# Optimization experiments

Hardware: AMD Instinct MI355X
Metric: run time of the kernel (lower is better)

The kernel has to match this reference:

```python
import jax, jax.numpy as jnp
import numpy as np

NFFT = 640
HOP = 320
REF_CH = 3  # reference microphone index


def _hann(n):
    # periodic Hann, matches torch.hann_window(n)
    return 0.5 * (1.0 - jnp.cos(2.0 * jnp.pi * jnp.arange(n, dtype=jnp.float32) / n))


def _stft(x):
    # x: [..., T] -> complex [..., F, Tf], center=True, constant (zero) pad
    win = _hann(NFFT)
    pad = NFFT // 2
    xp = jnp.pad(x, [(0, 0)] * (x.ndim - 1) + [(pad, pad)])
    T = x.shape[-1]
    nf = 1 + T // HOP
    idx = jnp.arange(nf)[:, None] * HOP + jnp.arange(NFFT)[None, :]
    frames = xp[..., idx] * win  # [..., Tf, NFFT]
    return jnp.swapaxes(jnp.fft.rfft(frames, axis=-1), -1, -2)  # [..., F, Tf]


def _istft(S):
    # S: [..., F, Tf] complex -> real [..., (Tf-1)*HOP]
    win = _hann(NFFT)
    frames = jnp.fft.irfft(jnp.swapaxes(S, -1, -2), n=NFFT, axis=-1) * win
    Tf = S.shape[-1]
    L = (Tf - 1) * HOP + NFFT
    idx = jnp.arange(Tf)[:, None] * HOP + jnp.arange(NFFT)[None, :]
    out = jnp.zeros(S.shape[:-2] + (L,), frames.dtype).at[..., idx].add(frames)
    wsum = jnp.zeros((L,), frames.dtype).at[idx].add(win * win)
    out = out / jnp.where(wsum > 1e-11, wsum, 1.0)
    p = NFFT // 2
    return out[..., p:L - p]


def _cov_features(xb):
    # xb: [C, T] -> [C*(C+1) + 2, F, Tf]
    S = _stft(xb)  # [C, F, Tf] complex
    C = xb.shape[0]
    iu, ju = np.triu_indices(C)  # upper triangle, row-major (matches torch mask order)
    cov = S[iu] * jnp.conj(S[ju])  # [C*(C+1)/2, F, Tf], cov[i,j] = S_i * conj(S_j)
    nF, nT = S.shape[-2], S.shape[-1]
    cov_ri = jnp.stack([cov.real, cov.imag], axis=1).reshape(-1, nF, nT)  # interleave re/im
    ref = S[REF_CH]
    return jnp.concatenate([cov_ri, ref.real[None], ref.imag[None]], axis=0)


def _forward(x, rtf_g, ref_g):
    B, C, T = x.shape
    feats = jax.vmap(_cov_features)(x)  # [B, 74, F, Tf]
    # STFT of generated reference channel
    refS = _stft(ref_g.reshape(B, -1))  # [B, F, Tf] complex
    nF, nT = refS.shape[-2], refS.shape[-1]
    # deep-filtering: unfold kernel (3,9) with padding (1,4) over (freq, frame)
    rp = jnp.pad(refS, ((0, 0), (1, 1), (4, 4)))
    patches = jnp.stack([rp[:, ki:ki + nF, kj:kj + nT]
                         for ki in range(3) for kj in range(9)], axis=1)  # [B, 27, F, Tf]
    rtf_c = (rtf_g[..., 0] + 1j * rtf_g[..., 1]).reshape(B, C - 1, 27, nF, nT)
    est = jnp.einsum('bmkft,bkft->bmft', rtf_c, patches)  # [B, C-1, F, Tf]
    est_audio = _istft(est.reshape(B * (C - 1), nF, nT)).reshape(B, C - 1, -1)
    valid = min(est_audio.shape[-1], ref_g.shape[-1])
    all_ch = jnp.concatenate([est_audio[:, :REF_CH, :valid],
                              ref_g[..., :valid],
                              est_audio[:, REF_CH:, :valid]], axis=1)  # [B, C, valid]
    return all_ch[0].T, feats


def setup_inputs() -> dict:
    key = jax.random.key(0)
    k1, k2, k3 = jax.random.split(key, 3)
    B, C, T = 2, 8, 96000
    nF, nT = NFFT // 2 + 1, 1 + T // HOP  # 321, 301
    x = jax.random.normal(k1, (B, C, T), dtype=jnp.float32)
    rtf_g = jax.random.normal(k2, (B, C - 1, 3, 9, nF, nT, 2), dtype=jnp.float32) * 0.1
    ref_g = jax.random.normal(k3, (B, 1, T), dtype=jnp.float32)
    return {"x": x, "rtf_g": rtf_g, "ref_g": ref_g}


def reference(x, rtf_g, ref_g):
    return _forward(x, rtf_g, ref_g)
```

## Files before the change

kernel.cpp:

```cpp
#include <hip/hip_runtime.h>
#include <math.h>

#define TLEN 96000
#define NFFT 640
#define HOP  320
#define NF   321
#define NT   301
#define FT   (NF * NT)

#define TWO_PI_F 6.28318530717958647692f

__constant__ int IU[36] = {0,0,0,0,0,0,0,0, 1,1,1,1,1,1,1, 2,2,2,2,2,2,
                           3,3,3,3,3, 4,4,4,4, 5,5,5, 6,6, 7};
__constant__ int JU[36] = {0,1,2,3,4,5,6,7, 1,2,3,4,5,6,7, 2,3,4,5,6,7,
                           3,4,5,6,7, 4,5,6,7, 5,6,7, 6,7, 7};

__global__ __launch_bounds__(192) void k_stft(const float* __restrict__ x,
                                              const float* __restrict__ ref_g,
                                              float2* __restrict__ Sx,
                                              float2* __restrict__ refS) {
    const int f   = blockIdx.x;
    const int s   = blockIdx.y;
    const int tid = threadIdx.x;

    __shared__ __align__(16) float2 ff[320];

    const float* sig = (s < 16) ? (x + (size_t)s * TLEN) : ref_g;
    for (int n = tid; n < 320; n += 192) {
        const int p0 = f * HOP + n - HOP;
        const int p1 = p0 + 320;
        const float c = cosf((TWO_PI_F / NFFT) * (float)n);
        float v0 = (p0 >= 0 && p0 < TLEN) ? sig[p0] : 0.0f;
        float v1 = (p1 < TLEN) ? sig[p1] : 0.0f;
        v0 *= (0.5f - 0.5f * c);
        v1 *= (0.5f + 0.5f * c);
        float2 o; o.x = v0 + v1; o.y = v0 - v1;
        ff[n] = o;
    }
    __syncthreads();

    if (tid < 161) {
        const int ke = 2 * tid;
        const int ko = ke + 1;
        const float we = (TWO_PI_F / NFFT) * (float)ke;
        const float wo = (TWO_PI_F / NFFT) * (float)ko;
        const float c2e = 2.0f * cosf(we);
        const float c2o = 2.0f * cosf(wo);

        float se1 = 0.0f, se2 = 0.0f, so1 = 0.0f, so2 = 0.0f;
#pragma unroll 8
        for (int n = 0; n < 320; ++n) {
            const float2 v = ff[n];
            const float te = fmaf(c2e, se1, v.x - se2); se2 = se1; se1 = te;
            const float to = fmaf(c2o, so1, v.y - so2); so2 = so1; so1 = to;
        }

        float sE, cE; sincosf(we, &sE, &cE);
        float sO, cO; sincosf(wo, &sO, &cO);
        float2 Xe, Xo;
        Xe.x = cE * se1 - se2;
        Xe.y = sE * se1;
        Xo.x = -(cO * so1 - so2);
        Xo.y = -(sO * so1);

        if (s < 16) {
            float2* base = Sx + (size_t)s * FT;
            base[(size_t)ke * NT + f] = Xe;
            if (ko < 320) base[(size_t)ko * NT + f] = Xo;
        } else {
            refS[(size_t)ke * NT + f] = Xe;
            if (ko < 320) refS[(size_t)ko * NT + f] = Xo;
        }
    }
}

__global__ void k_cov(const float2* __restrict__ Sx, float* __restrict__ feats) {
    int idx = blockIdx.x * blockDim.x + threadIdx.x;
    if (idx >= 2 * 37 * FT) return;
    const int kt  = idx % FT;
    const int job = (idx / FT) % 37;
    const int b   = idx / (37 * FT);
    const float2* Sb = Sx + (size_t)b * 8 * FT;
    float* fb = feats + (size_t)b * 74 * FT;
    if (job == 36) {
        const float2 r = Sb[(size_t)3 * FT + kt];
        fb[(size_t)72 * FT + kt] = r.x;
        fb[(size_t)73 * FT + kt] = r.y;
    } else {
        const float2 a = Sb[(size_t)IU[job] * FT + kt];
        const float2 c = Sb[(size_t)JU[job] * FT + kt];
        fb[(size_t)(2 * job)     * FT + kt] = a.x * c.x + a.y * c.y;
        fb[(size_t)(2 * job + 1) * FT + kt] = a.y * c.x - a.x * c.y;
    }
}

__global__ void k_dfilter(const float2* __restrict__ rtf,
                          const float2* __restrict__ refS,
                          float2* __restrict__ est) {
    int idx = blockIdx.x * blockDim.x + threadIdx.x;
    if (idx >= 7 * FT) return;
    const int t = idx % NT;
    const int f = (idx / NT) % NF;
    const int m = idx / FT;
    float er = 0.0f, ei = 0.0f;
#pragma unroll
    for (int ki = 0; ki < 3; ++ki) {
        const int ff = f + ki - 1;
#pragma unroll
        for (int kj = 0; kj < 9; ++kj) {
            const int tt = t + kj - 4;
            float pr = 0.0f, pi = 0.0f;
            if ((unsigned)ff < (unsigned)NF && (unsigned)tt < (unsigned)NT) {
                const float2 p = refS[(size_t)ff * NT + tt];
                pr = p.x; pi = p.y;
            }
            const float2 r = rtf[(size_t)(((m * 3 + ki) * 9 + kj) * NF + f) * NT + t];
            er = fmaf(r.x, pr, er); er = fmaf(-r.y, pi, er);
            ei = fmaf(r.x, pi, ei); ei = fmaf( r.y, pr, ei);
        }
    }
    float2 o; o.x = er; o.y = ei;
    est[idx] = o;
}

__global__ __launch_bounds__(320) void k_iframes(const float2* __restrict__ est,
                                                 float* __restrict__ frames) {
    const int f   = blockIdx.x;
    const int m   = blockIdx.y;
    const int tid = threadIdx.x;
    __shared__ __align__(16) float2 X[322];
    for (int k = tid; k < NF; k += 320)
        X[k] = est[((size_t)m * NF + k) * NT + f];
    if (tid == 0) { float2 z; z.x = 0.0f; z.y = 0.0f; X[321] = z; }
    __syncthreads();

    const int n = tid;
    float sp, cp; sincosf((TWO_PI_F / NFFT) * (float)n, &sp, &cp);
    const float c2p = cp * cp - sp * sp;
    const float s2p = 2.0f * sp * cp;
    const float c2  = 2.0f * c2p;

    float er1 = 0.0f, er2 = 0.0f, ei1 = 0.0f, ei2 = 0.0f;
    float or1 = 0.0f, or2 = 0.0f, oi1 = 0.0f, oi2 = 0.0f;
    const float4* Xp = (const float4*)X;
#pragma unroll 4
    for (int j = 0; j < 160; ++j) {
        const float4 v = Xp[j];
        const float t0 = fmaf(c2, er1, v.x - er2); er2 = er1; er1 = t0;
        const float t1 = fmaf(c2, ei1, v.y - ei2); ei2 = ei1; ei1 = t1;
        const float t2 = fmaf(c2, or1, v.z - or2); or2 = or1; or1 = t2;
        const float t3 = fmaf(c2, oi1, v.w - oi2); oi2 = oi1; oi1 = t3;
    }
    {
        const float4 v = Xp[160];
        const float t0 = fmaf(c2, er1, v.x - er2); er2 = er1; er1 = t0;
        const float t1 = fmaf(c2, ei1, v.y - ei2); ei2 = ei1; ei1 = t1;
    }

    const float PEbr = c2p * er1 + s2p * ei1 - er2;
    const float PEbi = c2p * ei1 - s2p * er1 - ei2;
    const float PObr = c2p * or1 + s2p * oi1 - or2;
    const float PObi = c2p * oi1 - s2p * or1 - oi2;

    float sr, crr; sincosf((TWO_PI_F / 320.0f) * (float)n, &sr, &crr);
    const float sgn  = (n & 1) ? -1.0f : 1.0f;
    const float RePE = sgn * (crr * PEbr - sr * PEbi);
    const float RePO = sgn * (cp * PObr - sp * PObi);

    const float base = X[0].x + sgn * X[320].x;
    const float y1 = 2.0f * (RePE + RePO) - base;
    const float y2 = 2.0f * (RePE - RePO) - base;

    const float w0 = 0.5f - 0.5f * cp;
    const float w1 = 0.5f + 0.5f * cp;
    const float inv = 1.0f / NFFT;
    float* fb = frames + ((size_t)m * NT + f) * NFFT;
    fb[n]       = y1 * inv * w0;
    fb[n + 320] = y2 * inv * w1;
}

__global__ void k_ola(const float* __restrict__ frames,
                      const float* __restrict__ ref_g,
                      float* __restrict__ out0) {
    int idx = blockIdx.x * blockDim.x + threadIdx.x;
    if (idx >= 8 * TLEN) return;
    const int c = idx & 7;
    const int t = idx >> 3;
    float o;
    if (c == 3) {
        o = ref_g[t];
    } else {
        const int m  = (c < 3) ? c : (c - 1);
        const int f1 = t / HOP + 1;
        const int n1 = t % HOP;
        const float a = frames[((size_t)m * NT + f1)     * NFFT + n1];
        const float b = frames[((size_t)m * NT + f1 - 1) * NFFT + n1 + 320];
        const float cw = cosf((TWO_PI_F / NFFT) * (float)n1);
        const float w0 = 0.5f - 0.5f * cw;
        const float w1 = 0.5f + 0.5f * cw;
        float ws = w0 * w0 + w1 * w1;
        ws = (ws > 1e-11f) ? ws : 1.0f;
        o = (a + b) / ws;
    }
    out0[idx] = o;
}

extern "C" void kernel_launch(void* const* d_in, const int* in_sizes, int n_in,
                              void* d_out, int out_size, void* d_ws, size_t ws_size,
                              hipStream_t stream) {
    const float* x     = (const float*)d_in[0];
    const float* rtf   = (const float*)d_in[1];
    const float* ref_g = (const float*)d_in[2];

    float* out0  = (float*)d_out;
    float* feats = (float*)d_out + (size_t)8 * TLEN;

    float2* Sx     = (float2*)d_ws;
    float2* refS   = Sx + (size_t)16 * FT;
    float2* est    = refS + (size_t)FT;
    float*  frames = (float*)(est + (size_t)7 * FT);

    k_stft<<<dim3(NT, 17), 192, 0, stream>>>(x, ref_g, Sx, refS);
    {
        const int total = 2 * 37 * FT;
        k_cov<<<(total + 255) / 256, 256, 0, stream>>>(Sx, feats);
    }
    {
        const int total = 7 * FT;
        k_dfilter<<<(total + 255) / 256, 256, 0, stream>>>(
            (const float2*)rtf, refS, est);
    }
    k_iframes<<<dim3(NT, 7), 320, 0, stream>>>(est, frames);
    {
        const int total = 8 * TLEN;
        k_ola<<<(total + 255) / 256, 256, 0, stream>>>(frames, ref_g, out0);
    }
}
```

Baseline: 469.6 us.

## Replace Goertzel DFTs with shared-memory mixed-radix FFT320 in STFT and iSTFT

Both the forward STFT and the inverse frame synthesis now pack the real 640-point transform into a 320-point complex FFT. That FFT is done as one radix-5 stage followed by radix-2 stages in shared memory, with a post- or pre-processing twiddle step to split and merge even and odd parts. This replaces the O(N^2) Goertzel recurrences, which ran about 320 serial FMAs per thread per bin, with O(N log N) work. In exchange it adds several __syncthreads barriers per block and uses fast __sincosf intrinsics, which may slightly reduce accuracy.

```diff
diff --git a/kernel.cpp b/kernel.cpp
--- a/kernel.cpp
+++ b/kernel.cpp
@@ -8,12 +8,99 @@
 #define NT   301
 #define FT   (NF * NT)
 
+#define PI_F     3.14159265358979323846f
 #define TWO_PI_F 6.28318530717958647692f
+
+#define CD640 0.99995180909f
+#define SD640 0.00981731938f
+
+#define C5_1 0.30901699437494742f
+#define S5_1 0.95105651629515357f
+#define C5_2 (-0.80901699437494742f)
+#define S5_2 0.58778525229247312f
 
 __constant__ int IU[36] = {0,0,0,0,0,0,0,0, 1,1,1,1,1,1,1, 2,2,2,2,2,2,
                            3,3,3,3,3, 4,4,4,4, 5,5,5, 6,6, 7};
 __constant__ int JU[36] = {0,1,2,3,4,5,6,7, 1,2,3,4,5,6,7, 2,3,4,5,6,7,
                            3,4,5,6,7, 4,5,6,7, 5,6,7, 6,7, 7};
+
+__device__ __forceinline__ float2 cmulf2(float2 a, float2 b) {
+    float2 r; r.x = a.x * b.x - a.y * b.y; r.y = a.x * b.y + a.y * b.x; return r;
+}
+
+__device__ __forceinline__ void fft320(float2* A, float2* B, int tid) {
+    if (tid < 64) {
+        const int n2 = tid;
+        const float2 x0 = A[n2];
+        const float2 x1 = A[n2 + 64];
+        const float2 x2 = A[n2 + 128];
+        const float2 x3 = A[n2 + 192];
+        const float2 x4 = A[n2 + 256];
+        float2 t1; t1.x = x1.x + x4.x; t1.y = x1.y + x4.y;
+        float2 t2; t2.x = x2.x + x3.x; t2.y = x2.y + x3.y;
+        float2 t3; t3.x = x1.x - x4.x; t3.y = x1.y - x4.y;
+        float2 t4; t4.x = x2.x - x3.x; t4.y = x2.y - x3.y;
+        float2 u0; u0.x = x0.x + t1.x + t2.x; u0.y = x0.y + t1.y + t2.y;
+        float2 u1, u2, u3, u4;
+        u1.x = x0.x + C5_1 * t1.x + C5_2 * t2.x + S5_1 * t3.y + S5_2 * t4.y;
+        u1.y = x0.y + C5_1 * t1.y + C5_2 * t2.y - S5_1 * t3.x - S5_2 * t4.x;
+        u2.x = x0.x + C5_2 * t1.x + C5_1 * t2.x + S5_2 * t3.y - S5_1 * t4.y;
+        u2.y = x0.y + C5_2 * t1.y + C5_1 * t2.y - S5_2 * t3.x + S5_1 * t4.x;
+        u3.x = x0.x + C5_2 * t1.x + C5_1 * t2.x - S5_2 * t3.y + S5_1 * t4.y;
+        u3.y = x0.y + C5_2 * t1.y + C5_1 * t2.y + S5_2 * t3.x - S5_1 * t4.x;
+        u4.x = x0.x + C5_1 * t1.x + C5_2 * t2.x - S5_1 * t3.y - S5_2 * t4.y;
+        u4.y = x0.y + C5_1 * t1.y + C5_2 * t2.y + S5_1 * t3.x + S5_2 * t4.x;
+        float sn, cs;
+        __sincosf((TWO_PI_F / 320.0f) * (float)n2, &sn, &cs);
+        float2 w1; w1.x = cs; w1.y = -sn;
+        const float2 w2 = cmulf2(w1, w1);
+        const float2 w3 = cmulf2(w2, w1);
+        const float2 w4 = cmulf2(w2, w2);
+        B[n2]       = u0;
+        B[64 + n2]  = cmulf2(u1, w1);
+        B[128 + n2] = cmulf2(u2, w2);
+        B[192 + n2] = cmulf2(u3, w3);
+        B[256 + n2] = cmulf2(u4, w4);
+    }
+    __syncthreads();
+    float2* src = B;
+    float2* dst = A;
+#pragma unroll
+    for (int s = 0; s < 5; ++s) {
+        if (tid < 160) {
+            const int r  = tid >> 5;
+            const int b  = tid & 31;
+            const int m  = 1 << s;
+            const int kk = b & (m - 1);
+            const int jm = b - kk;
+            const int j  = b >> s;
+            const int base = r << 6;
+            const float2 c0 = src[base + b];
+            const float2 c1 = src[base + b + 32];
+            float2 sm; sm.x = c0.x + c1.x; sm.y = c0.y + c1.y;
+            float2 df; df.x = c0.x - c1.x; df.y = c0.y - c1.y;
+            float sn, cs;
+            __sincosf(PI_F * (float)j / (float)(32 >> s), &sn, &cs);
+            float2 w; w.x = cs; w.y = -sn;
+            dst[base + kk + 2 * jm]     = sm;
+            dst[base + kk + 2 * jm + m] = cmulf2(df, w);
+        }
+        __syncthreads();
+        float2* t = src; src = dst; dst = t;
+    }
+    if (tid < 160) {
+        const int r = tid >> 5;
+        const int b = tid & 31;
+        const int base = r << 6;
+        const float2 c0 = src[base + b];
+        const float2 c1 = src[base + b + 32];
+        float2 sm; sm.x = c0.x + c1.x; sm.y = c0.y + c1.y;
+        float2 df; df.x = c0.x - c1.x; df.y = c0.y - c1.y;
+        dst[5 * b + r]       = sm;
+        dst[5 * b + 160 + r] = df;
+    }
+    __syncthreads();
+}
 
 __global__ __launch_bounds__(192) void k_stft(const float* __restrict__ x,
                                               const float* __restrict__ ref_g,
@@ -23,54 +110,53 @@
     const int s   = blockIdx.y;
     const int tid = threadIdx.x;
 
-    __shared__ __align__(16) float2 ff[320];
+    __shared__ __align__(16) float2 A[320];
+    __shared__ __align__(16) float2 B[320];
 
     const float* sig = (s < 16) ? (x + (size_t)s * TLEN) : ref_g;
-    for (int n = tid; n < 320; n += 192) {
-        const int p0 = f * HOP + n - HOP;
-        const int p1 = p0 + 320;
-        const float c = cosf((TWO_PI_F / NFFT) * (float)n);
-        float v0 = (p0 >= 0 && p0 < TLEN) ? sig[p0] : 0.0f;
-        float v1 = (p1 < TLEN) ? sig[p1] : 0.0f;
-        v0 *= (0.5f - 0.5f * c);
-        v1 *= (0.5f + 0.5f * c);
-        float2 o; o.x = v0 + v1; o.y = v0 - v1;
-        ff[n] = o;
-    }
-    __syncthreads();
-
-    if (tid < 161) {
-        const int ke = 2 * tid;
-        const int ko = ke + 1;
-        const float we = (TWO_PI_F / NFFT) * (float)ke;
-        const float wo = (TWO_PI_F / NFFT) * (float)ko;
-        const float c2e = 2.0f * cosf(we);
-        const float c2o = 2.0f * cosf(wo);
-
-        float se1 = 0.0f, se2 = 0.0f, so1 = 0.0f, so2 = 0.0f;
-#pragma unroll 8
-        for (int n = 0; n < 320; ++n) {
-            const float2 v = ff[n];
-            const float te = fmaf(c2e, se1, v.x - se2); se2 = se1; se1 = te;
-            const float to = fmaf(c2o, so1, v.y - so2); so2 = so1; so1 = to;
+
+    if (tid < 160) {
+#pragma unroll
+        for (int h = 0; h < 2; ++h) {
+            const int n = tid + 160 * h;
+            const int p = f * HOP - HOP + 2 * n;
+            const float v0 = (p >= 0 && p < TLEN) ? sig[p] : 0.0f;
+            const float v1 = (p >= -1 && p + 1 < TLEN) ? sig[p + 1] : 0.0f;
+            float sn, cs;
+            __sincosf((PI_F / 160.0f) * (float)n, &sn, &cs);
+            const float w0  = 0.5f - 0.5f * cs;
+            const float cs1 = cs * CD640 - sn * SD640;
+            const float w1  = 0.5f - 0.5f * cs1;
+            float2 z; z.x = v0 * w0; z.y = v1 * w1;
+            A[n] = z;
         }
-
-        float sE, cE; sincosf(we, &sE, &cE);
-        float sO, cO; sincosf(wo, &sO, &cO);
-        float2 Xe, Xo;
-        Xe.x = cE * se1 - se2;
-        Xe.y = sE * se1;
-        Xo.x = -(cO * so1 - so2);
-        Xo.y = -(sO * so1);
-
-        if (s < 16) {
-            float2* base = Sx + (size_t)s * FT;
-            base[(size_t)ke * NT + f] = Xe;
-            if (ko < 320) base[(size_t)ko * NT + f] = Xo;
-        } else {
-            refS[(size_t)ke * NT + f] = Xe;
-            if (ko < 320) refS[(size_t)ko * NT + f] = Xo;
-        }
+    }
+    __syncthreads();
+
+    fft320(A, B, tid);
+
+    if (tid <= 160) {
+        const int k  = tid;
+        const int kp = 320 - k;
+        const int km = (k == 0) ? 0 : kp;
+        const float2 Zk = B[k];
+        float2 Zc = B[km]; Zc.y = -Zc.y;
+        const float Er = 0.5f * (Zk.x + Zc.x);
+        const float Ei = 0.5f * (Zk.y + Zc.y);
+        const float Dr = 0.5f * (Zk.x - Zc.x);
+        const float Di = 0.5f * (Zk.y - Zc.y);
+        const float Gr = Di, Gi = -Dr;
+        float sp, cp;
+        __sincosf((PI_F / 320.0f) * (float)k, &sp, &cp);
+        float2 Xk;
+        Xk.x = Er + cp * Gr + sp * Gi;
+        Xk.y = Ei + cp * Gi - sp * Gr;
+        float2 Xp;
+        Xp.x =  Er - (cp * Di - sp * Dr);
+        Xp.y = -Ei - (cp * Dr + sp * Di);
+        float2* base = (s < 16) ? (Sx + (size_t)s * FT) : refS;
+        base[(size_t)k  * NT + f] = Xk;
+        base[(size_t)kp * NT + f] = Xp;
     }
 }
 
@@ -128,55 +214,55 @@
     const int f   = blockIdx.x;
     const int m   = blockIdx.y;
     const int tid = threadIdx.x;
-    __shared__ __align__(16) float2 X[322];
-    for (int k = tid; k < NF; k += 320)
-        X[k] = est[((size_t)m * NF + k) * NT + f];
-    if (tid == 0) { float2 z; z.x = 0.0f; z.y = 0.0f; X[321] = z; }
-    __syncthreads();
-
-    const int n = tid;
-    float sp, cp; sincosf((TWO_PI_F / NFFT) * (float)n, &sp, &cp);
-    const float c2p = cp * cp - sp * sp;
-    const float s2p = 2.0f * sp * cp;
-    const float c2  = 2.0f * c2p;
-
-    float er1 = 0.0f, er2 = 0.0f, ei1 = 0.0f, ei2 = 0.0f;
-    float or1 = 0.0f, or2 = 0.0f, oi1 = 0.0f, oi2 = 0.0f;
-    const float4* Xp = (const float4*)X;
-#pragma unroll 4
-    for (int j = 0; j < 160; ++j) {
-        const float4 v = Xp[j];
-        const float t0 = fmaf(c2, er1, v.x - er2); er2 = er1; er1 = t0;
-        const float t1 = fmaf(c2, ei1, v.y - ei2); ei2 = ei1; ei1 = t1;
-        const float t2 = fmaf(c2, or1, v.z - or2); or2 = or1; or1 = t2;
-        const float t3 = fmaf(c2, oi1, v.w - oi2); oi2 = oi1; oi1 = t3;
-    }
-    {
-        const float4 v = Xp[160];
-        const float t0 = fmaf(c2, er1, v.x - er2); er2 = er1; er1 = t0;
-        const float t1 = fmaf(c2, ei1, v.y - ei2); ei2 = ei1; ei1 = t1;
-    }
-
-    const float PEbr = c2p * er1 + s2p * ei1 - er2;
-    const float PEbi = c2p * ei1 - s2p * er1 - ei2;
-    const float PObr = c2p * or1 + s2p * oi1 - or2;
-    const float PObi = c2p * oi1 - s2p * or1 - oi2;
-
-    float sr, crr; sincosf((TWO_PI_F / 320.0f) * (float)n, &sr, &crr);
-    const float sgn  = (n & 1) ? -1.0f : 1.0f;
-    const float RePE = sgn * (crr * PEbr - sr * PEbi);
-    const float RePO = sgn * (cp * PObr - sp * PObi);
-
-    const float base = X[0].x + sgn * X[320].x;
-    const float y1 = 2.0f * (RePE + RePO) - base;
-    const float y2 = 2.0f * (RePE - RePO) - base;
-
-    const float w0 = 0.5f - 0.5f * cp;
-    const float w1 = 0.5f + 0.5f * cp;
-    const float inv = 1.0f / NFFT;
-    float* fb = frames + ((size_t)m * NT + f) * NFFT;
-    fb[n]       = y1 * inv * w0;
-    fb[n + 320] = y2 * inv * w1;
+
+    __shared__ __align__(16) float2 Xs[322];
+    __shared__ __align__(16) float2 A[320];
+    __shared__ __align__(16) float2 B[320];
+
+    {
+        const float2* eb = est + (size_t)m * NF * NT + f;
+        Xs[tid] = eb[(size_t)tid * NT];
+        if (tid == 0) Xs[320] = eb[(size_t)320 * NT];
+    }
+    __syncthreads();
+
+    if (tid <= 160) {
+        const int k = tid;
+        const float2 Xk = Xs[k];
+        const float2 X2 = Xs[320 - k];
+        const float Er = 0.5f * (Xk.x + X2.x);
+        const float Ei = 0.5f * (Xk.y - X2.y);
+        const float Hr = 0.5f * (Xk.x - X2.x);
+        const float Hi = 0.5f * (Xk.y + X2.y);
+        float sp, cp;
+        __sincosf((PI_F / 320.0f) * (float)k, &sp, &cp);
+        const float Or = cp * Hr - sp * Hi;
+        const float Oi = cp * Hi + sp * Hr;
+        float2 vk;
+        vk.x = Er - Oi; vk.y = -(Ei + Or);
+        A[k] = vk;
+        if (k >= 1 && k <= 159) {
+            float2 vp; vp.x = Er + Oi; vp.y = Ei - Or;
+            A[320 - k] = vp;
+        }
+    }
+    __syncthreads();
+
+    fft320(A, B, tid);
+
+    {
+        const int n = tid;
+        const float2 w = B[n];
+        float sn, cs;
+        __sincosf((PI_F / 160.0f) * (float)n, &sn, &cs);
+        const float w0  = 0.5f - 0.5f * cs;
+        const float cs1 = cs * CD640 - sn * SD640;
+        const float w1  = 0.5f - 0.5f * cs1;
+        const float inv = 1.0f / 320.0f;
+        float2 o; o.x = w.x * inv * w0; o.y = -w.y * inv * w1;
+        float* fb = frames + ((size_t)m * NT + f) * NFFT;
+        *(float2*)(fb + 2 * n) = o;
+    }
 }
 
 __global__ void k_ola(const float* __restrict__ frames,
```

After: 428.4 us. -8.8%, faster.
